# Optimization experiments

Hardware: AMD Instinct MI355X
Metric: run time of the kernel (lower is better)

Reference implementation:

```python
import jax, jax.numpy as jnp
import numpy as np

INT_STEPS = 7      # number of scaling-and-squaring steps
OUT_TIME_PT = 1.0  # integration end time


def _trilinear_sample(vol, locs):
    """Trilinear interpolation of vol at float voxel coords locs ('ij' indexing).
    vol:  [D, H, W, C]
    locs: [D, H, W, 3]
    returns [D, H, W, C]
    """
    D, H, W, _ = vol.shape
    max_idx = jnp.array([D - 1, H - 1, W - 1], dtype=locs.dtype)
    locs = jnp.clip(locs, 0.0, max_idx)
    l0 = jnp.floor(locs)
    w = locs - l0  # fractional weights in [0,1)
    i0 = l0.astype(jnp.int32)
    i1 = jnp.minimum(i0 + 1, max_idx.astype(jnp.int32))

    x0, y0, z0 = i0[..., 0], i0[..., 1], i0[..., 2]
    x1, y1, z1 = i1[..., 0], i1[..., 1], i1[..., 2]
    wx, wy, wz = w[..., 0:1], w[..., 1:2], w[..., 2:3]

    def g(x, y, z):
        return vol[x, y, z]  # advanced-index gather -> [D, H, W, C]

    # interpolate along z, then y, then x
    c00 = g(x0, y0, z0) * (1.0 - wz) + g(x0, y0, z1) * wz
    c01 = g(x0, y1, z0) * (1.0 - wz) + g(x0, y1, z1) * wz
    c10 = g(x1, y0, z0) * (1.0 - wz) + g(x1, y0, z1) * wz
    c11 = g(x1, y1, z0) * (1.0 - wz) + g(x1, y1, z1) * wz
    c0 = c00 * (1.0 - wy) + c01 * wy
    c1 = c10 * (1.0 - wy) + c11 * wy
    return c0 * (1.0 - wx) + c1 * wx


def _warp(vol, disp):
    """Linear warp: sample vol at identity grid + disp."""
    D, H, W, _ = vol.shape
    grid = jnp.stack(
        jnp.meshgrid(jnp.arange(D), jnp.arange(H), jnp.arange(W), indexing='ij'),
        axis=-1,
    ).astype(vol.dtype)  # [D, H, W, 3]
    return _trilinear_sample(vol, grid + disp)


def _integrate_ss(vel):
    """Scaling-and-squaring integration of a single velocity field [D,H,W,3]."""
    v = vel * (OUT_TIME_PT / (2.0 ** INT_STEPS))
    for _ in range(INT_STEPS):  # fixed small loop over squaring steps
        v = v + _warp(v, v)     # compose flow with itself
    return v


def setup_inputs() -> dict:
    key = jax.random.key(0)
    # stationary velocity field: [B, D, H, W, ndims=3]
    vel = jax.random.normal(key, (2, 160, 192, 160, 3), dtype=jnp.float32)
    return {"vel": vel}


def reference(vel):
    return jax.vmap(_integrate_ss)(vel)
```

## Files before the change

### kernel.cpp

```cpp
#include <hip/hip_runtime.h>


#define DD 160
#define HH 192
#define WW 160
#define VOX (DD * HH * WW)
#define NB 2
#define FIELD (VOX * 3)

struct __attribute__((packed, aligned(4))) pf4 { float x, y, z, w; };
struct __attribute__((packed, aligned(4))) pf2 { float x, y; };

__launch_bounds__(256)
__global__ void step_kernel(const float* __restrict__ src,
                            float* __restrict__ dst, float s) {
    int idx = blockIdx.x * 256 + threadIdx.x;
    if (idx >= NB * VOX) return;
    int b  = idx / VOX;
    int r  = idx - b * VOX;
    int d  = r / (HH * WW);
    int r2 = r - d * (HH * WW);
    int h  = r2 / WW;
    int w  = r2 - h * WW;

    const float* __restrict__ v = src + (size_t)b * FIELD;
    float* __restrict__ o       = dst + (size_t)b * FIELD;

    pf2 sl = *(const pf2*)(v + r * 3);
    float rv0 = sl.x, rv1 = sl.y;
    float rv2 = v[r * 3 + 2];

    float x = fminf(fmaxf((float)d + s * rv0, 0.0f), (float)(DD - 1));
    float y = fminf(fmaxf((float)h + s * rv1, 0.0f), (float)(HH - 1));
    float z = fminf(fmaxf((float)w + s * rv2, 0.0f), (float)(WW - 1));

    float xf = floorf(x), yf = floorf(y), zf = floorf(z);
    int x0 = (int)xf, y0 = (int)yf, z0 = (int)zf;
    int x1 = min(x0 + 1, DD - 1);
    int y1 = min(y0 + 1, HH - 1);
    float wx = x - xf, wy = y - yf, wz = z - zf;
    float iwx = 1.0f - wx, iwy = 1.0f - wy, iwz = 1.0f - wz;

    int zb = min(z0, WW - 2);
    bool sel = (z0 > zb);

    int ro00 = ((x0 * HH + y0) * WW + zb) * 3;
    int ro01 = ((x0 * HH + y1) * WW + zb) * 3;
    int ro10 = ((x1 * HH + y0) * WW + zb) * 3;
    int ro11 = ((x1 * HH + y1) * WW + zb) * 3;

    pf4 a00 = *(const pf4*)(v + ro00); pf2 b00 = *(const pf2*)(v + ro00 + 4);
    pf4 a01 = *(const pf4*)(v + ro01); pf2 b01 = *(const pf2*)(v + ro01 + 4);
    pf4 a10 = *(const pf4*)(v + ro10); pf2 b10 = *(const pf2*)(v + ro10 + 4);
    pf4 a11 = *(const pf4*)(v + ro11); pf2 b11 = *(const pf2*)(v + ro11 + 4);

    float g000 = sel ? a00.w : a00.x, g001 = sel ? b00.x : a00.y, g002 = sel ? b00.y : a00.z;
    float g010 = sel ? a01.w : a01.x, g011 = sel ? b01.x : a01.y, g012 = sel ? b01.y : a01.z;
    float g100 = sel ? a10.w : a10.x, g101 = sel ? b10.x : a10.y, g102 = sel ? b10.y : a10.z;
    float g110 = sel ? a11.w : a11.x, g111 = sel ? b11.x : a11.y, g112 = sel ? b11.y : a11.z;

    float out0, out1, out2;
    {
        float c00 = g000 * iwz + a00.w * wz;
        float c01 = g010 * iwz + a01.w * wz;
        float c10 = g100 * iwz + a10.w * wz;
        float c11 = g110 * iwz + a11.w * wz;
        float c0 = c00 * iwy + c01 * wy;
        float c1 = c10 * iwy + c11 * wy;
        out0 = s * (rv0 + (c0 * iwx + c1 * wx));
    }
    {
        float c00 = g001 * iwz + b00.x * wz;
        float c01 = g011 * iwz + b01.x * wz;
        float c10 = g101 * iwz + b10.x * wz;
        float c11 = g111 * iwz + b11.x * wz;
        float c0 = c00 * iwy + c01 * wy;
        float c1 = c10 * iwy + c11 * wy;
        out1 = s * (rv1 + (c0 * iwx + c1 * wx));
    }
    {
        float c00 = g002 * iwz + b00.y * wz;
        float c01 = g012 * iwz + b01.y * wz;
        float c10 = g102 * iwz + b10.y * wz;
        float c11 = g112 * iwz + b11.y * wz;
        float c0 = c00 * iwy + c01 * wy;
        float c1 = c10 * iwy + c11 * wy;
        out2 = s * (rv2 + (c0 * iwx + c1 * wx));
    }

    pf2 st; st.x = out0; st.y = out1;
    *(pf2*)(o + r * 3) = st;
    o[r * 3 + 2] = out2;
}

extern "C" void kernel_launch(void* const* d_in, const int* in_sizes, int n_in,
                              void* d_out, int out_size, void* d_ws, size_t ws_size,
                              hipStream_t stream) {
    const float* vel = (const float*)d_in[0];
    float* out = (float*)d_out;
    float* ws  = (float*)d_ws;

    const int nthreads = NB * VOX;
    const int blocks = (nthreads + 255) / 256;

    step_kernel<<<blocks, 256, 0, stream>>>(vel, out, 1.0f / 128.0f);
    step_kernel<<<blocks, 256, 0, stream>>>(out, ws, 1.0f);
    step_kernel<<<blocks, 256, 0, stream>>>(ws, out, 1.0f);
    step_kernel<<<blocks, 256, 0, stream>>>(out, ws, 1.0f);
    step_kernel<<<blocks, 256, 0, stream>>>(ws, out, 1.0f);
    step_kernel<<<blocks, 256, 0, stream>>>(out, ws, 1.0f);
    step_kernel<<<blocks, 256, 0, stream>>>(ws, out, 1.0f);
}
```

Baseline: 755.9 us.

## Pad velocity field to float4 layout for aligned trilinear gathers

```diff
diff --git a/kernel.cpp b/kernel.cpp
--- a/kernel.cpp
+++ b/kernel.cpp
@@ -7,9 +7,108 @@
 #define VOX (DD * HH * WW)
 #define NB 2
 #define FIELD (VOX * 3)
+#define PADBYTES ((size_t)NB * VOX * 16)
 
 struct __attribute__((packed, aligned(4))) pf4 { float x, y, z, w; };
 struct __attribute__((packed, aligned(4))) pf2 { float x, y; };
+
+__launch_bounds__(256)
+__global__ void conv_kernel(const float* __restrict__ src,
+                            float4* __restrict__ dst) {
+    int idx = blockIdx.x * 256 + threadIdx.x;
+    if (idx >= NB * VOX) return;
+    const float* p = src + (size_t)idx * 3;
+    float4 v;
+    v.x = p[0]; v.y = p[1]; v.z = p[2]; v.w = 0.0f;
+    dst[idx] = v;
+}
+
+template <bool OUT_PACKED>
+__launch_bounds__(256)
+__global__ void step_pad(const float4* __restrict__ src,
+                         float* __restrict__ dst, float s) {
+    int idx = blockIdx.x * 256 + threadIdx.x;
+    if (idx >= NB * VOX) return;
+    int b  = idx / VOX;
+    int r  = idx - b * VOX;
+    int d  = r / (HH * WW);
+    int r2 = r - d * (HH * WW);
+    int h  = r2 / WW;
+    int w  = r2 - h * WW;
+
+    const float4* __restrict__ v = src + (size_t)b * VOX;
+
+    float4 sv = v[r];
+
+    float x = fminf(fmaxf((float)d + s * sv.x, 0.0f), (float)(DD - 1));
+    float y = fminf(fmaxf((float)h + s * sv.y, 0.0f), (float)(HH - 1));
+    float z = fminf(fmaxf((float)w + s * sv.z, 0.0f), (float)(WW - 1));
+
+    float xf = floorf(x), yf = floorf(y), zf = floorf(z);
+    int x0 = (int)xf, y0 = (int)yf, z0 = (int)zf;
+    int x1 = min(x0 + 1, DD - 1);
+    int y1 = min(y0 + 1, HH - 1);
+    float wx = x - xf, wy = y - yf, wz = z - zf;
+    float iwx = 1.0f - wx, iwy = 1.0f - wy, iwz = 1.0f - wz;
+
+    int zb = min(z0, WW - 2);
+    bool sel = (z0 > zb);
+
+    int ro00 = (x0 * HH + y0) * WW + zb;
+    int ro01 = (x0 * HH + y1) * WW + zb;
+    int ro10 = (x1 * HH + y0) * WW + zb;
+    int ro11 = (x1 * HH + y1) * WW + zb;
+
+    float4 p00a = v[ro00], p00b = v[ro00 + 1];
+    float4 p01a = v[ro01], p01b = v[ro01 + 1];
+    float4 p10a = v[ro10], p10b = v[ro10 + 1];
+    float4 p11a = v[ro11], p11b = v[ro11 + 1];
+
+    float g000 = sel ? p00b.x : p00a.x, g001 = sel ? p00b.y : p00a.y, g002 = sel ? p00b.z : p00a.z;
+    float g010 = sel ? p01b.x : p01a.x, g011 = sel ? p01b.y : p01a.y, g012 = sel ? p01b.z : p01a.z;
+    float g100 = sel ? p10b.x : p10a.x, g101 = sel ? p10b.y : p10a.y, g102 = sel ? p10b.z : p10a.z;
+    float g110 = sel ? p11b.x : p11a.x, g111 = sel ? p11b.y : p11a.y, g112 = sel ? p11b.z : p11a.z;
+
+    float out0, out1, out2;
+    {
+        float c00 = g000 * iwz + p00b.x * wz;
+        float c01 = g010 * iwz + p01b.x * wz;
+        float c10 = g100 * iwz + p10b.x * wz;
+        float c11 = g110 * iwz + p11b.x * wz;
+        float c0 = c00 * iwy + c01 * wy;
+        float c1 = c10 * iwy + c11 * wy;
+        out0 = s * (sv.x + (c0 * iwx + c1 * wx));
+    }
+    {
+        float c00 = g001 * iwz + p00b.y * wz;
+        float c01 = g011 * iwz + p01b.y * wz;
+        float c10 = g101 * iwz + p10b.y * wz;
+        float c11 = g111 * iwz + p11b.y * wz;
+        float c0 = c00 * iwy + c01 * wy;
+        float c1 = c10 * iwy + c11 * wy;
+        out1 = s * (sv.y + (c0 * iwx + c1 * wx));
+    }
+    {
+        float c00 = g002 * iwz + p00b.z * wz;
+        float c01 = g012 * iwz + p01b.z * wz;
+        float c10 = g102 * iwz + p10b.z * wz;
+        float c11 = g112 * iwz + p11b.z * wz;
+        float c0 = c00 * iwy + c01 * wy;
+        float c1 = c10 * iwy + c11 * wy;
+        out2 = s * (sv.z + (c0 * iwx + c1 * wx));
+    }
+
+    if (OUT_PACKED) {
+        float* o = dst + (size_t)b * FIELD + (size_t)r * 3;
+        pf2 st; st.x = out0; st.y = out1;
+        *(pf2*)o = st;
+        o[2] = out2;
+    } else {
+        float4* o = (float4*)dst + (size_t)b * VOX + r;
+        float4 t; t.x = out0; t.y = out1; t.z = out2; t.w = 0.0f;
+        *o = t;
+    }
+}
 
 __launch_bounds__(256)
 __global__ void step_kernel(const float* __restrict__ src,
@@ -98,16 +197,29 @@
                               hipStream_t stream) {
     const float* vel = (const float*)d_in[0];
     float* out = (float*)d_out;
-    float* ws  = (float*)d_ws;
 
     const int nthreads = NB * VOX;
     const int blocks = (nthreads + 255) / 256;
 
-    step_kernel<<<blocks, 256, 0, stream>>>(vel, out, 1.0f / 128.0f);
-    step_kernel<<<blocks, 256, 0, stream>>>(out, ws, 1.0f);
-    step_kernel<<<blocks, 256, 0, stream>>>(ws, out, 1.0f);
-    step_kernel<<<blocks, 256, 0, stream>>>(out, ws, 1.0f);
-    step_kernel<<<blocks, 256, 0, stream>>>(ws, out, 1.0f);
-    step_kernel<<<blocks, 256, 0, stream>>>(out, ws, 1.0f);
-    step_kernel<<<blocks, 256, 0, stream>>>(ws, out, 1.0f);
-}
+    if (ws_size >= 2 * PADBYTES) {
+        float4* A = (float4*)d_ws;
+        float4* B = A + (size_t)NB * VOX;
+        conv_kernel<<<blocks, 256, 0, stream>>>(vel, A);
+        step_pad<false><<<blocks, 256, 0, stream>>>(A, (float*)B, 1.0f / 128.0f);
+        step_pad<false><<<blocks, 256, 0, stream>>>(B, (float*)A, 1.0f);
+        step_pad<false><<<blocks, 256, 0, stream>>>(A, (float*)B, 1.0f);
+        step_pad<false><<<blocks, 256, 0, stream>>>(B, (float*)A, 1.0f);
+        step_pad<false><<<blocks, 256, 0, stream>>>(A, (float*)B, 1.0f);
+        step_pad<false><<<blocks, 256, 0, stream>>>(B, (float*)A, 1.0f);
+        step_pad<true ><<<blocks, 256, 0, stream>>>(A, out, 1.0f);
+    } else {
+        float* ws = (float*)d_ws;
+        step_kernel<<<blocks, 256, 0, stream>>>(vel, out, 1.0f / 128.0f);
+        step_kernel<<<blocks, 256, 0, stream>>>(out, ws, 1.0f);
+        step_kernel<<<blocks, 256, 0, stream>>>(ws, out, 1.0f);
+        step_kernel<<<blocks, 256, 0, stream>>>(out, ws, 1.0f);
+        step_kernel<<<blocks, 256, 0, stream>>>(ws, out, 1.0f);
+        step_kernel<<<blocks, 256, 0, stream>>>(out, ws, 1.0f);
+        step_kernel<<<blocks, 256, 0, stream>>>(ws, out, 1.0f);
+    }
+}
```

After: 1.097 ms. 45.1% more time.
